# Optimization experiments

Measured on AMD Instinct MI355X. Metric: run time of the kernel, lower is better.

Reference implementation:

```python
import jax, jax.numpy as jnp
import numpy as np

B, S, D = 2, 2048, 2048
H, KV, HD = 32, 8, 64          # n_heads, n_kv_heads, head_dim
REP = H // KV                   # GQA repeat factor
NEG = -1e30                     # causal mask fill


def setup_inputs() -> dict:
    key = jax.random.key(0)
    ks = jax.random.split(key, 5)
    x = jax.random.normal(ks[0], (B, S, D), dtype=jnp.float32)
    # llama rotary frequencies: theta = 10000^{-2i/hd}
    inv_freq = 1.0 / (10000.0 ** (np.arange(0, HD, 2, dtype=np.float32) / HD))
    angles = np.outer(np.arange(S, dtype=np.float32), inv_freq)  # (S, HD/2)
    freqs_cos = jnp.asarray(np.cos(angles), dtype=jnp.float32)
    freqs_sin = jnp.asarray(np.sin(angles), dtype=jnp.float32)
    sc = 0.02
    wq = jax.random.normal(ks[1], (H * HD, D), dtype=jnp.float32) * sc
    wk = jax.random.normal(ks[2], (KV * HD, D), dtype=jnp.float32) * sc
    wv = jax.random.normal(ks[3], (KV * HD, D), dtype=jnp.float32) * sc
    wo = jax.random.normal(ks[4], (D, H * HD), dtype=jnp.float32) * sc
    return {"x": x, "freqs_cos": freqs_cos, "freqs_sin": freqs_sin,
            "wq": wq, "wk": wk, "wv": wv, "wo": wo}


def _rope(t, cos, sin):
    # t: (B, S, h, HD); even/odd lanes form (real, imag) pairs
    tr, ti = t[..., 0::2], t[..., 1::2]
    cos = cos[None, :, None, :]
    sin = sin[None, :, None, :]
    out_r = tr * cos - ti * sin
    out_i = tr * sin + ti * cos
    return jnp.stack([out_r, out_i], axis=-1).reshape(t.shape)


def reference(x, freqs_cos, freqs_sin, wq, wk, wv, wo):
    # QKV projections (torch Linear convention: y = x @ W.T)
    q = (x @ wq.T).reshape(B, S, H, HD)
    k = (x @ wk.T).reshape(B, S, KV, HD)
    v = (x @ wv.T).reshape(B, S, KV, HD)
    q = _rope(q, freqs_cos, freqs_sin)
    k = _rope(k, freqs_cos, freqs_sin)
    # GQA: group query heads instead of materializing repeat_kv
    q = q.transpose(0, 2, 1, 3).reshape(B, KV, REP, S, HD)  # (B,g,r,S,HD)
    k = k.transpose(0, 2, 1, 3)                              # (B,g,S,HD)
    v = v.transpose(0, 2, 1, 3)                              # (B,g,S,HD)
    scores = jnp.einsum('bgrqh,bgkh->bgrqk', q, k) / np.float32(np.sqrt(HD))
    causal = jnp.tril(jnp.ones((S, S), dtype=bool))
    scores = jnp.where(causal[None, None, None], scores, NEG)
    probs = jax.nn.softmax(scores, axis=-1)
    out = jnp.einsum('bgrqk,bgkh->bgrqh', probs, v)
    out = out.reshape(B, H, S, HD).transpose(0, 2, 1, 3).reshape(B, S, H * HD)
    return out @ wo.T
```

## Files before the change

kernel.cpp:

```cpp
#include <hip/hip_runtime.h>
#include <stdint.h>

#define S_LEN 2048
#define D_DIM 2048
#define NH 32
#define NKV 8
#define HD 64
#define B_SZ 2
#define QKV_N 3072
#define K_OFF 2048
#define V_OFF 2560
#define SCL 0.1803368801111244f

typedef unsigned short ushort_t;
typedef __attribute__((ext_vector_type(8))) short short8;
typedef __attribute__((ext_vector_type(4))) float f32x4;
typedef __attribute__((ext_vector_type(16))) float f32x16;

#define SBAR() do { __builtin_amdgcn_sched_barrier(0); __builtin_amdgcn_s_barrier(); __builtin_amdgcn_sched_barrier(0); } while (0)
#define WAITV4() asm volatile("s_waitcnt vmcnt(4)" ::: "memory")
#define WAITV0() asm volatile("s_waitcnt vmcnt(0)" ::: "memory")

__device__ __forceinline__ float b2f(ushort_t u) {
  union { unsigned int i; float f; } x; x.i = ((unsigned int)u) << 16; return x.f;
}
__device__ __forceinline__ ushort_t f2b(float f) {
  union { float f; unsigned int i; } x; x.f = f;
  unsigned int r = x.i + 0x7FFFu + ((x.i >> 16) & 1u);
  return (ushort_t)(r >> 16);
}

__device__ __forceinline__ void load_lds16(const ushort_t* g, ushort_t* l) {
  __builtin_amdgcn_global_load_lds(
      (const __attribute__((address_space(1))) void*)g,
      (__attribute__((address_space(3))) void*)l, 16, 0, 0);
}

__device__ __forceinline__ short8 ld_swz(const ushort_t* base, int row, int colElem) {
  int byte = (row << 7) + (colElem << 1);
  byte ^= (row & 7) << 4;
  return *(const short8*)((const char*)base + byte);
}

__device__ __forceinline__ uint32_t cvtpk(float a, float b) {
  uint32_t r;
  asm("v_cvt_pk_bf16_f32 %0, %1, %2" : "=v"(r) : "v"(a), "v"(b));
  return r;
}
__device__ __forceinline__ void pswap(uint32_t& a, uint32_t& b) {
  asm("v_permlane32_swap_b32 %0, %1" : "+v"(a), "+v"(b));
}
__device__ __forceinline__ short8 mk8(uint32_t w0, uint32_t w1, uint32_t w2, uint32_t w3) {
  union { uint32_t w[4]; short8 v; } u;
  u.w[0] = w0; u.w[1] = w1; u.w[2] = w2; u.w[3] = w3;
  return u.v;
}

__global__ void cvt_bf16(const float* __restrict__ in, ushort_t* __restrict__ out, int n8) {
  int i = blockIdx.x * blockDim.x + threadIdx.x;
  if (i >= n8) return;
  const float4* p = (const float4*)(in + (size_t)i * 8);
  float4 x0 = p[0], x1 = p[1];
  ushort_t u[8] = { f2b(x0.x), f2b(x0.y), f2b(x0.z), f2b(x0.w),
                    f2b(x1.x), f2b(x1.y), f2b(x1.z), f2b(x1.w) };
  *(uint4*)(out + (size_t)i * 8) = *(const uint4*)u;
}

template <int HEADS, int LOG2H>
__global__ void rope_kernel(ushort_t* __restrict__ t, const float* __restrict__ cosT,
                            const float* __restrict__ sinT, int n8) {
  int idx = blockIdx.x * blockDim.x + threadIdx.x;
  if (idx >= n8) return;
  int d8 = idx & 7;
  int rest = idx >> 3;
  int h = rest & (HEADS - 1);
  int row = rest >> LOG2H;
  int s = row & (S_LEN - 1);
  float4 c4 = *(const float4*)(cosT + s * 32 + d8 * 4);
  float4 s4 = *(const float4*)(sinT + s * 32 + d8 * 4);
  ushort_t* p = t + (size_t)row * QKV_N + h * HD + d8 * 8;
  ushort_t u[8]; *(uint4*)u = *(const uint4*)p;
  float c[4] = { c4.x, c4.y, c4.z, c4.w }, sn[4] = { s4.x, s4.y, s4.z, s4.w };
  ushort_t o[8];
#pragma unroll
  for (int j = 0; j < 4; ++j) {
    float re = b2f(u[2 * j]), im = b2f(u[2 * j + 1]);
    o[2 * j]     = f2b(re * c[j] - im * sn[j]);
    o[2 * j + 1] = f2b(re * sn[j] + im * c[j]);
  }
  *(uint4*)p = *(const uint4*)o;
}

__global__ __launch_bounds__(256) void transpose_v(const ushort_t* __restrict__ v,
                                                   ushort_t* __restrict__ vt) {
  __shared__ ushort_t tile[64][80];
  int st = blockIdx.x, g = blockIdx.y, b = blockIdx.z;
  int tid = threadIdx.x;
#pragma unroll
  for (int p = 0; p < 2; ++p) {
    int o = p * 2048 + tid * 8;
    int s = o >> 6, d = o & 63;
    uint4 val = *(const uint4*)(v + ((size_t)(b * S_LEN + st * 64 + s) * QKV_N + g * HD + d));
    *(uint4*)&tile[s][d] = val;
  }
  __syncthreads();
#pragma unroll
  for (int p = 0; p < 2; ++p) {
    int o = p * 2048 + tid * 8;
    int d = o >> 6, s0 = o & 63;
    ushort_t tmp[8];
#pragma unroll
    for (int j = 0; j < 8; ++j) tmp[j] = tile[s0 + j][d];
    *(uint4*)(vt + (((size_t)(b * NKV + g) * HD + d) * S_LEN + st * 64 + s0)) = *(const uint4*)tmp;
  }
}

#define DSR(MH, NH) \
  _Pragma("unroll") for (int mi = 0; mi < 4; ++mi) \
    _Pragma("unroll") for (int ks = 0; ks < 2; ++ks) \
      af[mi][ks] = ld_swz(Ac, wr * 128 + ((MH) * 4 + mi) * 16 + l15, ks * 32 + lhi * 8); \
  _Pragma("unroll") for (int ni = 0; ni < 2; ++ni) \
    _Pragma("unroll") for (int ks = 0; ks < 2; ++ks) \
      bfr[ni][ks] = ld_swz(Bc, wc * 64 + ((NH) * 2 + ni) * 16 + l15, ks * 32 + lhi * 8);

#define MFM(MH, NH) \
  _Pragma("unroll") for (int mi = 0; mi < 4; ++mi) \
    _Pragma("unroll") for (int ni = 0; ni < 2; ++ni) \
      _Pragma("unroll") for (int ks = 0; ks < 2; ++ks) \
        acc[(MH) * 4 + mi][(NH) * 2 + ni] = __builtin_amdgcn_mfma_f32_16x16x32_bf16( \
            af[mi][ks], bfr[ni][ks], acc[(MH) * 4 + mi][(NH) * 2 + ni], 0, 0, 0);

template <typename OutT>
__global__ __launch_bounds__(512, 2) void gemm8_bt(const ushort_t* __restrict__ A,
                                                   const ushort_t* __restrict__ Bw,
                                                   OutT* __restrict__ C,
                                                   int M, int N, int K) {
  __shared__ ushort_t Ab[2][256 * 64];
  __shared__ ushort_t Bb[2][256 * 64];
  const int tid = threadIdx.x, lane = tid & 63, wave = tid >> 6;
  const int wr = wave >> 2, wc = wave & 3;
  const int l15 = lane & 15, lhi = lane >> 4;
  const int nwg = gridDim.x * gridDim.y;
  const int orig = blockIdx.y * gridDim.x + blockIdx.x;
  const int w = ((orig & 7) * (nwg >> 3)) + (orig >> 3);
  const size_t rb = (size_t)(w / gridDim.x) * 256;
  const size_t cb = (size_t)(w % gridDim.x) * 256;
  const int NK = K >> 6;

  auto stageA = [&](int kt, ushort_t* dst, int g) {
#pragma unroll
    for (int p = 0; p < 2; ++p) {
      const int ub = p * 16384 + g * 8192 + wave * 1024;
      const int lb = ub + lane * 16;
      const int row = lb >> 7;
      const int csw = ((lb & 127) ^ ((row & 7) << 4)) >> 1;
      load_lds16(A + (rb + row) * (size_t)K + kt * 64 + csw,
                 (ushort_t*)((char*)dst + ub));
    }
  };
  auto stageB = [&](int kt, ushort_t* dst, int g) {
#pragma unroll
    for (int p = 0; p < 2; ++p) {
      const int ub = p * 16384 + (wave >> 2) * 8192 + g * 4096 + (wave & 3) * 1024;
      const int lb = ub + lane * 16;
      const int row = lb >> 7;
      const int csw = ((lb & 127) ^ ((row & 7) << 4)) >> 1;
      load_lds16(Bw + (cb + row) * (size_t)K + kt * 64 + csw,
                 (ushort_t*)((char*)dst + ub));
    }
  };

  f32x4 acc[8][4];
#pragma unroll
  for (int i = 0; i < 8; ++i)
#pragma unroll
    for (int j = 0; j < 4; ++j) acc[i][j] = (f32x4){0.f, 0.f, 0.f, 0.f};

  stageA(0, Ab[0], 0); stageA(0, Ab[0], 1);
  stageB(0, Bb[0], 0); stageB(0, Bb[0], 1);
  stageA(1, Ab[1], 0); stageB(1, Bb[1], 0);
  WAITV4();
  SBAR();

  short8 af[4][2], bfr[2][2];
#pragma unroll 1
  for (int kt = 0; kt < NK; ++kt) {
    ushort_t* Ac = Ab[kt & 1];
    ushort_t* Bc = Bb[kt & 1];
    ushort_t* An = Ab[(kt & 1) ^ 1];
    ushort_t* Bn = Bb[(kt & 1) ^ 1];
    DSR(0, 0); if (kt + 1 < NK) stageA(kt + 1, An, 1);
    SBAR(); __builtin_amdgcn_s_setprio(1); MFM(0, 0); __builtin_amdgcn_s_setprio(0); SBAR();
    DSR(0, 1); if (kt + 1 < NK) stageB(kt + 1, Bn, 1);
    SBAR(); __builtin_amdgcn_s_setprio(1); MFM(0, 1); __builtin_amdgcn_s_setprio(0); SBAR();
    DSR(1, 0); if (kt + 2 < NK) stageA(kt + 2, Ac, 0);
    SBAR(); __builtin_amdgcn_s_setprio(1); MFM(1, 0); __builtin_amdgcn_s_setprio(0); SBAR();
    DSR(1, 1); if (kt + 2 < NK) stageB(kt + 2, Bc, 0);
    SBAR(); __builtin_amdgcn_s_setprio(1); MFM(1, 1); __builtin_amdgcn_s_setprio(0);
    if (kt + 2 < NK) { WAITV4(); } else if (kt + 1 < NK) { WAITV0(); }
    SBAR();
  }

#pragma unroll
  for (int m = 0; m < 8; ++m) {
    const size_t r0 = rb + wr * 128 + m * 16 + lhi * 4;
#pragma unroll
    for (int n = 0; n < 4; ++n) {
      const size_t c0 = cb + wc * 64 + n * 16 + l15;
#pragma unroll
      for (int r = 0; r < 4; ++r) {
        float v = acc[m][n][r];
        if constexpr (sizeof(OutT) == 2) C[(r0 + r) * N + c0] = f2b(v);
        else                             C[(r0 + r) * N + c0] = v;
      }
    }
  }
}

__global__ __launch_bounds__(256) void flash_attn(const ushort_t* __restrict__ q,
                                                  const ushort_t* __restrict__ k,
                                                  const ushort_t* __restrict__ vt,
                                                  ushort_t* __restrict__ out) {
  __shared__ ushort_t Ks[2][64 * 64];
  __shared__ ushort_t Vs[2][64 * 64];
  const int pairIdx = blockIdx.x, h = blockIdx.y, b = blockIdx.z;
  const int g = h >> 2;
  const int tid = threadIdx.x, lane = tid & 63, wave = tid >> 6;
  const int l31 = lane & 31, hi = lane >> 5;

  int srcRow[2], srcCol[2], ldsOff[2];
#pragma unroll
  for (int c = 0; c < 2; ++c) {
    const int o = c * 4096 + wave * 1024 + lane * 16;
    const int r = o >> 7;
    srcRow[c] = r;
    srcCol[c] = ((o & 127) ^ ((r & 7) << 4)) >> 1;
    ldsOff[c] = (c * 4096 + wave * 1024) / 2;
  }
  const ushort_t* kbase = k + (size_t)b * S_LEN * QKV_N + g * HD;
  const ushort_t* vbase = vt + (size_t)(b * NKV + g) * HD * S_LEN;

#pragma unroll 1
  for (int halfi = 0; halfi < 2; ++halfi) {
    const int qt = (halfi == 0) ? pairIdx : (15 - pairIdx);
    const int qwbase = qt * 128 + wave * 32;
    const int qglob = qwbase + l31;

    short8 qf[4];
    {
      const ushort_t* qp = q + (size_t)(b * S_LEN + qglob) * QKV_N + h * HD + hi * 8;
#pragma unroll
      for (int s = 0; s < 4; ++s) qf[s] = *(const short8*)(qp + s * 16);
    }
    f32x16 oacc[2];
#pragma unroll
    for (int d = 0; d < 2; ++d)
#pragma unroll
      for (int r = 0; r < 16; ++r) oacc[d][r] = 0.f;
    float msc = -3e38f, lrow = 0.f;

#pragma unroll
    for (int c = 0; c < 2; ++c) {
      load_lds16(kbase + (size_t)srcRow[c] * QKV_N + srcCol[c], &Ks[0][ldsOff[c]]);
      load_lds16(vbase + (size_t)srcRow[c] * S_LEN + srcCol[c], &Vs[0][ldsOff[c]]);
    }
    __syncthreads();

    int cur = 0;
    const int nt = 2 * (qt + 1);
    for (int t = 0; t < nt; ++t) {
      const int kv0 = t * 64;
      if (t + 1 < nt) {
        const int nk = kv0 + 64;
#pragma unroll
        for (int c = 0; c < 2; ++c) {
          load_lds16(kbase + (size_t)(nk + srcRow[c]) * QKV_N + srcCol[c], &Ks[cur ^ 1][ldsOff[c]]);
          load_lds16(vbase + (size_t)srcRow[c] * S_LEN + nk + srcCol[c], &Vs[cur ^ 1][ldsOff[c]]);
        }
      }
      if (kv0 <= qwbase + 31) {
        f32x16 pacc[2];
#pragma unroll
        for (int j = 0; j < 2; ++j) {
          f32x16 z;
#pragma unroll
          for (int r = 0; r < 16; ++r) z[r] = 0.f;
#pragma unroll
          for (int s = 0; s < 4; ++s) {
            short8 kf = ld_swz(Ks[cur], j * 32 + l31, s * 16 + hi * 8);
            z = __builtin_amdgcn_mfma_f32_32x32x16_bf16(kf, qf[s], z, 0, 0, 0);
          }
          pacc[j] = z;
        }
        if (kv0 + 63 > qwbase) {
#pragma unroll
          for (int j = 0; j < 2; ++j)
#pragma unroll
            for (int r = 0; r < 16; ++r) {
              const int kvabs = kv0 + j * 32 + (r & 3) + 8 * (r >> 2) + 4 * hi;
              pacc[j][r] = (kvabs <= qglob) ? pacc[j][r] : -1e30f;
            }
        }
        float mraw = -3e38f;
#pragma unroll
        for (int j = 0; j < 2; ++j)
#pragma unroll
          for (int r = 0; r < 16; ++r) mraw = fmaxf(mraw, pacc[j][r]);
        mraw = fmaxf(mraw, __shfl_xor(mraw, 32));
        const float mscn = fmaxf(msc, mraw * SCL);
        const float sold = exp2f(msc - mscn);
        msc = mscn;
        float rs = 0.f;
        short8 pf[4];
#pragma unroll
        for (int j = 0; j < 2; ++j) {
          float pv[16];
#pragma unroll
          for (int r = 0; r < 16; ++r) {
            pv[r] = exp2f(pacc[j][r] * SCL - msc);
            rs += pv[r];
          }
          uint32_t w0 = cvtpk(pv[0], pv[1]),  w1 = cvtpk(pv[2], pv[3]);
          uint32_t w2 = cvtpk(pv[4], pv[5]),  w3 = cvtpk(pv[6], pv[7]);
          uint32_t w4 = cvtpk(pv[8], pv[9]),  w5 = cvtpk(pv[10], pv[11]);
          uint32_t w6 = cvtpk(pv[12], pv[13]), w7 = cvtpk(pv[14], pv[15]);
          pswap(w0, w2); pswap(w1, w3); pswap(w4, w6); pswap(w5, w7);
          pf[2 * j]     = mk8(w0, w1, w2, w3);
          pf[2 * j + 1] = mk8(w4, w5, w6, w7);
        }
        rs += __shfl_xor(rs, 32);
        lrow = lrow * sold + rs;
#pragma unroll
        for (int dblk = 0; dblk < 2; ++dblk) {
#pragma unroll
          for (int r = 0; r < 16; ++r) oacc[dblk][r] *= sold;
#pragma unroll
          for (int s = 0; s < 4; ++s) {
            short8 vf = ld_swz(Vs[cur], dblk * 32 + l31, s * 16 + hi * 8);
            oacc[dblk] = __builtin_amdgcn_mfma_f32_32x32x16_bf16(vf, pf[s], oacc[dblk], 0, 0, 0);
          }
        }
      }
      __syncthreads();
      cur ^= 1;
    }
    const float inv = 1.f / lrow;
    ushort_t* op = out + (size_t)(b * S_LEN + qglob) * (NH * HD) + h * HD;
#pragma unroll
    for (int dblk = 0; dblk < 2; ++dblk) {
      float ov[16];
#pragma unroll
      for (int r = 0; r < 16; ++r) ov[r] = oacc[dblk][r] * inv;
      uint32_t w0 = cvtpk(ov[0], ov[1]),  w1 = cvtpk(ov[2], ov[3]);
      uint32_t w2 = cvtpk(ov[4], ov[5]),  w3 = cvtpk(ov[6], ov[7]);
      uint32_t w4 = cvtpk(ov[8], ov[9]),  w5 = cvtpk(ov[10], ov[11]);
      uint32_t w6 = cvtpk(ov[12], ov[13]), w7 = cvtpk(ov[14], ov[15]);
      pswap(w0, w2); pswap(w1, w3); pswap(w4, w6); pswap(w5, w7);
      uint4 stlo; stlo.x = w0; stlo.y = w1; stlo.z = w2; stlo.w = w3;
      uint4 sthi; sthi.x = w4; sthi.y = w5; sthi.z = w6; sthi.w = w7;
      *(uint4*)(op + dblk * 32 + hi * 8)      = stlo;
      *(uint4*)(op + dblk * 32 + 16 + hi * 8) = sthi;
    }
  }
}

extern "C" void kernel_launch(void* const* d_in, const int* in_sizes, int n_in,
                              void* d_out, int out_size, void* d_ws, size_t ws_size,
                              hipStream_t stream) {
  const float* x  = (const float*)d_in[0];
  const float* fc = (const float*)d_in[1];
  const float* fs = (const float*)d_in[2];
  const float* wq = (const float*)d_in[3];
  const float* wk = (const float*)d_in[4];
  const float* wv = (const float*)d_in[5];
  const float* wo = (const float*)d_in[6];
  float* out = (float*)d_out;
  ushort_t* ws = (ushort_t*)d_ws;

  const size_t n_x   = (size_t)B_SZ * S_LEN * D_DIM;
  const size_t n_wq  = (size_t)NH * HD * D_DIM;
  const size_t n_wk  = (size_t)NKV * HD * D_DIM;
  const size_t n_qkv = (size_t)B_SZ * S_LEN * QKV_N;
  const size_t n_q   = (size_t)B_SZ * S_LEN * NH * HD;
  const size_t n_k   = (size_t)B_SZ * S_LEN * NKV * HD;

  size_t off = 0;
  ushort_t* xb   = ws + off; off += n_x;
  ushort_t* wqb  = ws + off; off += n_wq;
  ushort_t* wkb  = ws + off; off += n_wk;
  ushort_t* wvb  = ws + off; off += n_wk;
  ushort_t* wob  = ws + off; off += n_wq;
  ushort_t* qkvb = ws + off; off += n_qkv;
  ushort_t* vtb  = ws + off; off += n_k;
  ushort_t* ab   = ws + off; off += n_q;
  (void)ws_size; (void)in_sizes; (void)n_in; (void)out_size;

  auto cvt = [&](const float* src, ushort_t* dst, size_t n) {
    int n8 = (int)(n / 8);
    cvt_bf16<<<dim3((n8 + 255) / 256), dim3(256), 0, stream>>>(src, dst, n8);
  };
  cvt(x, xb, n_x);
  cvt(wq, wqb, n_wq);
  cvt(wk, wkb, n_wk);
  cvt(wv, wvb, n_wk);
  cvt(wo, wob, n_wq);

  const int M = B_SZ * S_LEN;
  gemm8_bt<ushort_t><<<dim3(QKV_N / 256, M / 256), 512, 0, stream>>>(xb, wqb, qkvb, M, QKV_N, D_DIM);

  rope_kernel<NH, 5><<<dim3((M * NH * 8) / 256), 256, 0, stream>>>(qkvb, fc, fs, M * NH * 8);
  rope_kernel<NKV, 3><<<dim3((M * NKV * 8) / 256), 256, 0, stream>>>(qkvb + K_OFF, fc, fs, M * NKV * 8);

  transpose_v<<<dim3(S_LEN / 64, NKV, B_SZ), 256, 0, stream>>>(qkvb + V_OFF, vtb);

  flash_attn<<<dim3(8, NH, B_SZ), 256, 0, stream>>>(qkvb, qkvb + K_OFF, vtb, ab);

  gemm8_bt<float><<<dim3(D_DIM / 256, M / 256), 512, 0, stream>>>(ab, wob, out, M, D_DIM, D_DIM);
}
```

Measured before the change: 261.0 us.

## Remap flash attention to one GQA group per block and use smaller output GEMM

Flash attention now gives each block one 32-row query tile, with each of its four waves handling one of the four query heads that share a KV group. The K/V tiles in LDS are therefore reused across the heads of a group, and the grid grows to 64×8×2 blocks in reverse causal order in place of the paired-tile scheme. The output projection switches from the 256-tile gemm8_bt to a new simple 128-tile gemm_bt with single-buffered LDS and no swizzle. That raises block count but may lose the pipelining and bank-conflict avoidance of the original GEMM.

Result: slower. 279.0 us (+6.9%).

```diff
diff --git a/kernel.cpp b/kernel.cpp
--- a/kernel.cpp
+++ b/kernel.cpp
@@ -112,6 +112,66 @@
 #pragma unroll
     for (int j = 0; j < 8; ++j) tmp[j] = tile[s0 + j][d];
     *(uint4*)(vt + (((size_t)(b * NKV + g) * HD + d) * S_LEN + st * 64 + s0)) = *(const uint4*)tmp;
+  }
+}
+
+template <typename OutT>
+__global__ __launch_bounds__(256) void gemm_bt(const ushort_t* __restrict__ A,
+                                               const ushort_t* __restrict__ Bw,
+                                               OutT* __restrict__ C,
+                                               int M, int N, int K) {
+  __shared__ ushort_t As[128 * 32];
+  __shared__ ushort_t Bs[128 * 32];
+  const int tid = threadIdx.x;
+  const int lane = tid & 63, wave = tid >> 6;
+  const int wr = wave >> 1, wc = wave & 1;
+  const int nwg = gridDim.x * gridDim.y;
+  const int orig = blockIdx.y * gridDim.x + blockIdx.x;
+  const int w = ((orig & 7) * (nwg >> 3)) + (orig >> 3);
+  const size_t rb = (size_t)(w / gridDim.x) * 128;
+  const size_t cb = (size_t)(w % gridDim.x) * 128;
+  f32x4 acc[4][4];
+#pragma unroll
+  for (int i = 0; i < 4; ++i)
+#pragma unroll
+    for (int j = 0; j < 4; ++j) acc[i][j] = (f32x4){0.f, 0.f, 0.f, 0.f};
+
+  for (int k0 = 0; k0 < K; k0 += 32) {
+    __syncthreads();
+#pragma unroll
+    for (int c = 0; c < 2; ++c) {
+      const int o = c * 4096 + wave * 1024 + lane * 16;
+      const int r = o >> 6;
+      const int col = (o >> 1) & 31;
+      load_lds16(A + (rb + r) * K + k0 + col, As + (c * 4096 + wave * 1024) / 2);
+      load_lds16(Bw + (cb + r) * K + k0 + col, Bs + (c * 4096 + wave * 1024) / 2);
+    }
+    __syncthreads();
+    short8 a[4], b[4];
+#pragma unroll
+    for (int i = 0; i < 4; ++i) {
+      a[i] = *(const short8*)(As + (wr * 64 + i * 16 + (lane & 15)) * 32 + (lane >> 4) * 8);
+      b[i] = *(const short8*)(Bs + (wc * 64 + i * 16 + (lane & 15)) * 32 + (lane >> 4) * 8);
+    }
+#pragma unroll
+    for (int i = 0; i < 4; ++i)
+#pragma unroll
+      for (int j = 0; j < 4; ++j)
+        acc[i][j] = __builtin_amdgcn_mfma_f32_16x16x32_bf16(a[i], b[j], acc[i][j], 0, 0, 0);
+  }
+#pragma unroll
+  for (int i = 0; i < 4; ++i) {
+    const size_t r0 = rb + wr * 64 + i * 16 + ((lane >> 4) * 4);
+#pragma unroll
+    for (int j = 0; j < 4; ++j) {
+      const size_t c0 = cb + wc * 64 + j * 16 + (lane & 15);
+#pragma unroll
+      for (int r = 0; r < 4; ++r) {
+        float v = acc[i][j][r];
+        if constexpr (sizeof(OutT) == 2) C[(r0 + r) * N + c0] = f2b(v);
+        else                             C[(r0 + r) * N + c0] = v;
+      }
+    }
   }
 }
 
@@ -223,9 +283,10 @@
                                                   ushort_t* __restrict__ out) {
   __shared__ ushort_t Ks[2][64 * 64];
   __shared__ ushort_t Vs[2][64 * 64];
-  const int pairIdx = blockIdx.x, h = blockIdx.y, b = blockIdx.z;
-  const int g = h >> 2;
+  const int qt = 63 - blockIdx.x;
+  const int g = blockIdx.y, b = blockIdx.z;
   const int tid = threadIdx.x, lane = tid & 63, wave = tid >> 6;
+  const int h = g * 4 + wave;
   const int l31 = lane & 31, hi = lane >> 5;
 
   int srcRow[2], srcCol[2], ldsOff[2];
@@ -240,127 +301,121 @@
   const ushort_t* kbase = k + (size_t)b * S_LEN * QKV_N + g * HD;
   const ushort_t* vbase = vt + (size_t)(b * NKV + g) * HD * S_LEN;
 
-#pragma unroll 1
-  for (int halfi = 0; halfi < 2; ++halfi) {
-    const int qt = (halfi == 0) ? pairIdx : (15 - pairIdx);
-    const int qwbase = qt * 128 + wave * 32;
-    const int qglob = qwbase + l31;
-
-    short8 qf[4];
-    {
-      const ushort_t* qp = q + (size_t)(b * S_LEN + qglob) * QKV_N + h * HD + hi * 8;
-#pragma unroll
-      for (int s = 0; s < 4; ++s) qf[s] = *(const short8*)(qp + s * 16);
-    }
-    f32x16 oacc[2];
-#pragma unroll
-    for (int d = 0; d < 2; ++d)
-#pragma unroll
-      for (int r = 0; r < 16; ++r) oacc[d][r] = 0.f;
-    float msc = -3e38f, lrow = 0.f;
-
-#pragma unroll
-    for (int c = 0; c < 2; ++c) {
-      load_lds16(kbase + (size_t)srcRow[c] * QKV_N + srcCol[c], &Ks[0][ldsOff[c]]);
-      load_lds16(vbase + (size_t)srcRow[c] * S_LEN + srcCol[c], &Vs[0][ldsOff[c]]);
+  const int qwbase = qt * 32;
+  const int qglob = qwbase + l31;
+
+  short8 qf[4];
+  {
+    const ushort_t* qp = q + (size_t)(b * S_LEN + qglob) * QKV_N + h * HD + hi * 8;
+#pragma unroll
+    for (int s = 0; s < 4; ++s) qf[s] = *(const short8*)(qp + s * 16);
+  }
+  f32x16 oacc[2];
+#pragma unroll
+  for (int d = 0; d < 2; ++d)
+#pragma unroll
+    for (int r = 0; r < 16; ++r) oacc[d][r] = 0.f;
+  float msc = -3e38f, lrow = 0.f;
+
+#pragma unroll
+  for (int c = 0; c < 2; ++c) {
+    load_lds16(kbase + (size_t)srcRow[c] * QKV_N + srcCol[c], &Ks[0][ldsOff[c]]);
+    load_lds16(vbase + (size_t)srcRow[c] * S_LEN + srcCol[c], &Vs[0][ldsOff[c]]);
+  }
+  __syncthreads();
+
+  int cur = 0;
+  const int nt = (qt >> 1) + 1;
+  for (int t = 0; t < nt; ++t) {
+    const int kv0 = t * 64;
+    if (t + 1 < nt) {
+      const int nk = kv0 + 64;
+#pragma unroll
+      for (int c = 0; c < 2; ++c) {
+        load_lds16(kbase + (size_t)(nk + srcRow[c]) * QKV_N + srcCol[c], &Ks[cur ^ 1][ldsOff[c]]);
+        load_lds16(vbase + (size_t)srcRow[c] * S_LEN + nk + srcCol[c], &Vs[cur ^ 1][ldsOff[c]]);
+      }
+    }
+    f32x16 pacc[2];
+#pragma unroll
+    for (int j = 0; j < 2; ++j) {
+      f32x16 z;
+#pragma unroll
+      for (int r = 0; r < 16; ++r) z[r] = 0.f;
+#pragma unroll
+      for (int s = 0; s < 4; ++s) {
+        short8 kf = ld_swz(Ks[cur], j * 32 + l31, s * 16 + hi * 8);
+        z = __builtin_amdgcn_mfma_f32_32x32x16_bf16(kf, qf[s], z, 0, 0, 0);
+      }
+      pacc[j] = z;
+    }
+    if (kv0 + 63 > qwbase) {
+#pragma unroll
+      for (int j = 0; j < 2; ++j)
+#pragma unroll
+        for (int r = 0; r < 16; ++r) {
+          const int kvabs = kv0 + j * 32 + (r & 3) + 8 * (r >> 2) + 4 * hi;
+          pacc[j][r] = (kvabs <= qglob) ? pacc[j][r] : -1e30f;
+        }
+    }
+    float mraw = -3e38f;
+#pragma unroll
+    for (int j = 0; j < 2; ++j)
+#pragma unroll
+      for (int r = 0; r < 16; ++r) mraw = fmaxf(mraw, pacc[j][r]);
+    mraw = fmaxf(mraw, __shfl_xor(mraw, 32));
+    const float mscn = fmaxf(msc, mraw * SCL);
+    const float sold = exp2f(msc - mscn);
+    msc = mscn;
+    float rs = 0.f;
+    short8 pf[4];
+#pragma unroll
+    for (int j = 0; j < 2; ++j) {
+      float pv[16];
+#pragma unroll
+      for (int r = 0; r < 16; ++r) {
+        pv[r] = exp2f(pacc[j][r] * SCL - msc);
+        rs += pv[r];
+      }
+      uint32_t w0 = cvtpk(pv[0], pv[1]),  w1 = cvtpk(pv[2], pv[3]);
+      uint32_t w2 = cvtpk(pv[4], pv[5]),  w3 = cvtpk(pv[6], pv[7]);
+      uint32_t w4 = cvtpk(pv[8], pv[9]),  w5 = cvtpk(pv[10], pv[11]);
+      uint32_t w6 = cvtpk(pv[12], pv[13]), w7 = cvtpk(pv[14], pv[15]);
+      pswap(w0, w2); pswap(w1, w3); pswap(w4, w6); pswap(w5, w7);
+      pf[2 * j]     = mk8(w0, w1, w2, w3);
+      pf[2 * j + 1] = mk8(w4, w5, w6, w7);
+    }
+    rs += __shfl_xor(rs, 32);
+    lrow = lrow * sold + rs;
+#pragma unroll
+    for (int dblk = 0; dblk < 2; ++dblk) {
+#pragma unroll
+      for (int r = 0; r < 16; ++r) oacc[dblk][r] *= sold;
+#pragma unroll
+      for (int s = 0; s < 4; ++s) {
+        short8 vf = ld_swz(Vs[cur], dblk * 32 + l31, s * 16 + hi * 8);
+        oacc[dblk] = __builtin_amdgcn_mfma_f32_32x32x16_bf16(vf, pf[s], oacc[dblk], 0, 0, 0);
+      }
     }
     __syncthreads();
-
-    int cur = 0;
-    const int nt = 2 * (qt + 1);
-    for (int t = 0; t < nt; ++t) {
-      const int kv0 = t * 64;
-      if (t + 1 < nt) {
-        const int nk = kv0 + 64;
-#pragma unroll
-        for (int c = 0; c < 2; ++c) {
-          load_lds16(kbase + (size_t)(nk + srcRow[c]) * QKV_N + srcCol[c], &Ks[cur ^ 1][ldsOff[c]]);
-          load_lds16(vbase + (size_t)srcRow[c] * S_LEN + nk + srcCol[c], &Vs[cur ^ 1][ldsOff[c]]);
-        }
-      }
-      if (kv0 <= qwbase + 31) {
-        f32x16 pacc[2];
-#pragma unroll
-        for (int j = 0; j < 2; ++j) {
-          f32x16 z;
-#pragma unroll
-          for (int r = 0; r < 16; ++r) z[r] = 0.f;
-#pragma unroll
-          for (int s = 0; s < 4; ++s) {
-            short8 kf = ld_swz(Ks[cur], j * 32 + l31, s * 16 + hi * 8);
-            z = __builtin_amdgcn_mfma_f32_32x32x16_bf16(kf, qf[s], z, 0, 0, 0);
-          }
-          pacc[j] = z;
-        }
-        if (kv0 + 63 > qwbase) {
-#pragma unroll
-          for (int j = 0; j < 2; ++j)
-#pragma unroll
-            for (int r = 0; r < 16; ++r) {
-              const int kvabs = kv0 + j * 32 + (r & 3) + 8 * (r >> 2) + 4 * hi;
-              pacc[j][r] = (kvabs <= qglob) ? pacc[j][r] : -1e30f;
-            }
-        }
-        float mraw = -3e38f;
-#pragma unroll
-        for (int j = 0; j < 2; ++j)
-#pragma unroll
-          for (int r = 0; r < 16; ++r) mraw = fmaxf(mraw, pacc[j][r]);
-        mraw = fmaxf(mraw, __shfl_xor(mraw, 32));
-        const float mscn = fmaxf(msc, mraw * SCL);
-        const float sold = exp2f(msc - mscn);
-        msc = mscn;
-        float rs = 0.f;
-        short8 pf[4];
-#pragma unroll
-        for (int j = 0; j < 2; ++j) {
-          float pv[16];
-#pragma unroll
-          for (int r = 0; r < 16; ++r) {
-            pv[r] = exp2f(pacc[j][r] * SCL - msc);
-            rs += pv[r];
-          }
-          uint32_t w0 = cvtpk(pv[0], pv[1]),  w1 = cvtpk(pv[2], pv[3]);
-          uint32_t w2 = cvtpk(pv[4], pv[5]),  w3 = cvtpk(pv[6], pv[7]);
-          uint32_t w4 = cvtpk(pv[8], pv[9]),  w5 = cvtpk(pv[10], pv[11]);
-          uint32_t w6 = cvtpk(pv[12], pv[13]), w7 = cvtpk(pv[14], pv[15]);
-          pswap(w0, w2); pswap(w1, w3); pswap(w4, w6); pswap(w5, w7);
-          pf[2 * j]     = mk8(w0, w1, w2, w3);
-          pf[2 * j + 1] = mk8(w4, w5, w6, w7);
-        }
-        rs += __shfl_xor(rs, 32);
-        lrow = lrow * sold + rs;
-#pragma unroll
-        for (int dblk = 0; dblk < 2; ++dblk) {
-#pragma unroll
-          for (int r = 0; r < 16; ++r) oacc[dblk][r] *= sold;
-#pragma unroll
-          for (int s = 0; s < 4; ++s) {
-            short8 vf = ld_swz(Vs[cur], dblk * 32 + l31, s * 16 + hi * 8);
-            oacc[dblk] = __builtin_amdgcn_mfma_f32_32x32x16_bf16(vf, pf[s], oacc[dblk], 0, 0, 0);
-          }
-        }
-      }
-      __syncthreads();
-      cur ^= 1;
-    }
-    const float inv = 1.f / lrow;
-    ushort_t* op = out + (size_t)(b * S_LEN + qglob) * (NH * HD) + h * HD;
-#pragma unroll
-    for (int dblk = 0; dblk < 2; ++dblk) {
-      float ov[16];
-#pragma unroll
-      for (int r = 0; r < 16; ++r) ov[r] = oacc[dblk][r] * inv;
-      uint32_t w0 = cvtpk(ov[0], ov[1]),  w1 = cvtpk(ov[2], ov[3]);
-      uint32_t w2 = cvtpk(ov[4], ov[5]),  w3 = cvtpk(ov[6], ov[7]);
-      uint32_t w4 = cvtpk(ov[8], ov[9]),  w5 = cvtpk(ov[10], ov[11]);
-      uint32_t w6 = cvtpk(ov[12], ov[13]), w7 = cvtpk(ov[14], ov[15]);
-      pswap(w0, w2); pswap(w1, w3); pswap(w4, w6); pswap(w5, w7);
-      uint4 stlo; stlo.x = w0; stlo.y = w1; stlo.z = w2; stlo.w = w3;
-      uint4 sthi; sthi.x = w4; sthi.y = w5; sthi.z = w6; sthi.w = w7;
-      *(uint4*)(op + dblk * 32 + hi * 8)      = stlo;
-      *(uint4*)(op + dblk * 32 + 16 + hi * 8) = sthi;
-    }
+    cur ^= 1;
+  }
+  const float inv = 1.f / lrow;
+  ushort_t* op = out + (size_t)(b * S_LEN + qglob) * (NH * HD) + h * HD;
+#pragma unroll
+  for (int dblk = 0; dblk < 2; ++dblk) {
+    float ov[16];
+#pragma unroll
+    for (int r = 0; r < 16; ++r) ov[r] = oacc[dblk][r] * inv;
+    uint32_t w0 = cvtpk(ov[0], ov[1]),  w1 = cvtpk(ov[2], ov[3]);
+    uint32_t w2 = cvtpk(ov[4], ov[5]),  w3 = cvtpk(ov[6], ov[7]);
+    uint32_t w4 = cvtpk(ov[8], ov[9]),  w5 = cvtpk(ov[10], ov[11]);
+    uint32_t w6 = cvtpk(ov[12], ov[13]), w7 = cvtpk(ov[14], ov[15]);
+    pswap(w0, w2); pswap(w1, w3); pswap(w4, w6); pswap(w5, w7);
+    uint4 stlo; stlo.x = w0; stlo.y = w1; stlo.z = w2; stlo.w = w3;
+    uint4 sthi; sthi.x = w4; sthi.y = w5; sthi.z = w6; sthi.w = w7;
+    *(uint4*)(op + dblk * 32 + hi * 8)      = stlo;
+    *(uint4*)(op + dblk * 32 + 16 + hi * 8) = sthi;
   }
 }
 
@@ -413,7 +468,7 @@
 
   transpose_v<<<dim3(S_LEN / 64, NKV, B_SZ), 256, 0, stream>>>(qkvb + V_OFF, vtb);
 
-  flash_attn<<<dim3(8, NH, B_SZ), 256, 0, stream>>>(qkvb, qkvb + K_OFF, vtb, ab);
-
-  gemm8_bt<float><<<dim3(D_DIM / 256, M / 256), 512, 0, stream>>>(ab, wob, out, M, D_DIM, D_DIM);
-}
+  flash_attn<<<dim3(64, NKV, B_SZ), 256, 0, stream>>>(qkvb, qkvb + K_OFF, vtb, ab);
+
+  gemm_bt<float><<<dim3(D_DIM / 128, M / 128), 256, 0, stream>>>(ab, wob, out, M, D_DIM, D_DIM);
+}
```
